# Performance work log

Hardware: AMD Instinct MI355X
Metric: run time of the kernel (lower is better)

Reference implementation:

```python
import jax, jax.numpy as jnp
import numpy as np

S, B, D, H, E, HID = 512, 16, 768, 12, 8, 3072
HD = D // H
EPS = 1e-5


def _ln(x, w, b):
    m = jnp.mean(x, axis=-1, keepdims=True)
    v = jnp.var(x, axis=-1, keepdims=True)
    return (x - m) * jax.lax.rsqrt(v + EPS) * w + b


def setup_inputs() -> dict:
    key = jax.random.key(0)
    ks = jax.random.split(key, 9)
    n = lambda k, *sh: jax.random.normal(k, sh, dtype=jnp.float32) * 0.02
    return dict(
        x=jax.random.normal(ks[0], (S, B, D), dtype=jnp.float32),
        ln1_w=jnp.ones((D,), jnp.float32), ln1_b=jnp.zeros((D,), jnp.float32),
        wq=n(ks[1], D, D), bq=jnp.zeros((D,), jnp.float32),
        wk=n(ks[2], D, D), bk=jnp.zeros((D,), jnp.float32),
        wv=n(ks[3], D, D), bv=jnp.zeros((D,), jnp.float32),
        wo=n(ks[4], D, D), bo=jnp.zeros((D,), jnp.float32),
        ln2_w=jnp.ones((D,), jnp.float32), ln2_b=jnp.zeros((D,), jnp.float32),
        wg=n(ks[5], D, E), bg=jnp.zeros((E,), jnp.float32),
        w1=n(ks[6], E, D, HID), b1=jnp.zeros((E, HID), jnp.float32),
        w2=n(ks[7], E, HID, D), b2=jnp.zeros((E, D), jnp.float32),
    )


def _block(x, ln1_w, ln1_b, wq, bq, wk, bk, wv, bv, wo, bo,
           ln2_w, ln2_b, wg, bg, w1, b1, w2, b2):
    # --- attention: source uses query = norm1(x), key = value = x ---
    q_in = _ln(x, ln1_w, ln1_b)
    q = (q_in @ wq + bq).reshape(S, B, H, HD)
    k = (x @ wk + bk).reshape(S, B, H, HD)
    v = (x @ wv + bv).reshape(S, B, H, HD)
    scores = jnp.einsum('sbhd,tbhd->bhst', q, k) * (1.0 / HD ** 0.5)
    p = jax.nn.softmax(scores, axis=-1)
    attn = jnp.einsum('bhst,tbhd->sbhd', p, v).reshape(S, B, D)
    x = x + attn @ wo + bo
    # --- top-1 MoE MLP on norm2(x) ---
    t = _ln(x, ln2_w, ln2_b).reshape(S * B, D)   # [T, D] routed tokens
    logits = t @ wg + bg                          # [T, E]
    probs = jax.nn.softmax(logits, axis=-1)
    idx = jnp.argmax(logits, axis=-1)             # top-1 expert per token
    gate = jnp.take_along_axis(probs, idx[:, None], axis=-1)   # [T, 1]
    comb = jax.nn.one_hot(idx, E, dtype=t.dtype) * gate        # [T, E]

    def expert(w1e, b1e, w2e, b2e):
        return jax.nn.gelu(t @ w1e + b1e, approximate=False) @ w2e + b2e

    y = jax.vmap(expert)(w1, b1, w2, b2)          # [E, T, D]
    moe = jnp.einsum('te,etd->td', comb, y).reshape(S, B, D)
    return x + moe


def reference(x, ln1_w, ln1_b, wq, bq, wk, bk, wv, bv, wo, bo,
              ln2_w, ln2_b, wg, bg, w1, b1, w2, b2):
    return _block(x, ln1_w, ln1_b, wq, bq, wk, bk, wv, bv, wo, bo,
                  ln2_w, ln2_b, wg, bg, w1, b1, w2, b2)
```

## Files before the change

kernel.cpp:

```cpp
#include <hip/hip_runtime.h>
#include <math.h>

#define SS 512
#define BB 16
#define DD 768
#define HH 12
#define HDIM 64
#define EE 8
#define HID 3072
#define TT 8192
#define EPSV 1e-5f
#define KVSTR 1536
#define ASTR 72
#define NBANK 64

typedef __attribute__((ext_vector_type(8))) short s16x8;
typedef __attribute__((ext_vector_type(4))) short s16x4;
typedef __attribute__((ext_vector_type(4))) float f32x4;

__device__ inline short f2bf(float f) {
  unsigned u = __builtin_bit_cast(unsigned, f);
  unsigned r = (u + 0x7fffu + ((u >> 16) & 1u)) >> 16;
  return (short)r;
}

__device__ inline float gelu_f(float x) {
  float y = 0.7978845608028654f * (x + 0.044715f * x * x * x);
  float e = __expf(2.f * y);
  float t = 1.f - 2.f / (e + 1.f);
  return 0.5f * x * (1.f + t);
}

__device__ inline void gl2lds16(const void* g, void* l) {
  __builtin_amdgcn_global_load_lds(
      (const __attribute__((address_space(1))) unsigned int*)g,
      (__attribute__((address_space(3))) unsigned int*)l, 16, 0, 0);
}

__global__ __launch_bounds__(256) void transpose4_bf16(const float* __restrict__ w0,
    const float* __restrict__ w1p, const float* __restrict__ w2p,
    const float* __restrict__ w3p, short* __restrict__ dst) {
  const int z = blockIdx.z;
  const float* W = (z == 0) ? w0 : (z == 1) ? w1p : (z == 2) ? w2p : w3p;
  short* Wt = dst + (size_t)z * DD * DD;
  int k0 = blockIdx.x * 64, n0 = blockIdx.y * 64;
  __shared__ float t[64][65];
  for (int i = threadIdx.x; i < 1024; i += 256) {
    int r = i >> 4, c4 = (i & 15) << 2;
    const float4 v = *(const float4*)(W + (size_t)(k0 + r) * DD + n0 + c4);
    t[r][c4] = v.x; t[r][c4 + 1] = v.y; t[r][c4 + 2] = v.z; t[r][c4 + 3] = v.w;
  }
  __syncthreads();
  for (int i = threadIdx.x; i < 1024; i += 256) {
    int r = i >> 4, c4 = (i & 15) << 2;
    s16x4 sv;
    sv.x = f2bf(t[c4][r]);     sv.y = f2bf(t[c4 + 1][r]);
    sv.z = f2bf(t[c4 + 2][r]); sv.w = f2bf(t[c4 + 3][r]);
    *(s16x4*)(Wt + (size_t)(n0 + r) * DD + k0 + c4) = sv;
  }
}

__global__ __launch_bounds__(256) void transpose_bf16(const float* __restrict__ W,
    short* __restrict__ Wt, int K, int N) {
  const float* Wz = W + (size_t)blockIdx.z * K * N;
  short* Wtz = Wt + (size_t)blockIdx.z * K * N;
  int k0 = blockIdx.x * 64, n0 = blockIdx.y * 64;
  __shared__ float t[64][65];
  for (int i = threadIdx.x; i < 1024; i += 256) {
    int r = i >> 4, c4 = (i & 15) << 2;
    const float4 v = *(const float4*)(Wz + (size_t)(k0 + r) * N + n0 + c4);
    t[r][c4] = v.x; t[r][c4 + 1] = v.y; t[r][c4 + 2] = v.z; t[r][c4 + 3] = v.w;
  }
  __syncthreads();
  for (int i = threadIdx.x; i < 1024; i += 256) {
    int r = i >> 4, c4 = (i & 15) << 2;
    s16x4 sv;
    sv.x = f2bf(t[c4][r]);     sv.y = f2bf(t[c4 + 1][r]);
    sv.z = f2bf(t[c4 + 2][r]); sv.w = f2bf(t[c4 + 3][r]);
    *(s16x4*)(Wtz + (size_t)(n0 + r) * K + k0 + c4) = sv;
  }
}

__global__ __launch_bounds__(256) void gate_transpose(const float* __restrict__ wg,
    float* __restrict__ wgT) {
  for (int i = threadIdx.x + blockIdx.x * 256; i < EE * DD; i += 256 * 8) {
    int e = i / DD, d = i - e * DD;
    wgT[i] = wg[d * EE + e];
  }
}

__global__ __launch_bounds__(256) void fused_cvt_ln1(const float* __restrict__ x,
    const float* __restrict__ w, const float* __restrict__ b,
    short* __restrict__ xbf, short* __restrict__ ln1bf) {
  const int tok = blockIdx.x * 4 + (threadIdx.x >> 6);
  const int lane = threadIdx.x & 63;
  const float* row = x + (size_t)tok * DD;
  const float4 v0 = *(const float4*)(row + lane * 4);
  const float4 v1 = *(const float4*)(row + 256 + lane * 4);
  const float4 v2 = *(const float4*)(row + 512 + lane * 4);
  float s = v0.x + v0.y + v0.z + v0.w + v1.x + v1.y + v1.z + v1.w
          + v2.x + v2.y + v2.z + v2.w;
  float ss = v0.x * v0.x + v0.y * v0.y + v0.z * v0.z + v0.w * v0.w
           + v1.x * v1.x + v1.y * v1.y + v1.z * v1.z + v1.w * v1.w
           + v2.x * v2.x + v2.y * v2.y + v2.z * v2.z + v2.w * v2.w;
#pragma unroll
  for (int o = 1; o < 64; o <<= 1) { s += __shfl_xor(s, o); ss += __shfl_xor(ss, o); }
  const float mean = s * (1.f / DD);
  const float inv = rsqrtf(ss * (1.f / DD) - mean * mean + EPSV);
  short* xrow = xbf + (size_t)tok * DD;
  short* lrow = ln1bf + (size_t)tok * DD;
#define LN1_CHUNK(v, off) { \
  const float4 wv = *(const float4*)(w + (off) + lane * 4); \
  const float4 bv = *(const float4*)(b + (off) + lane * 4); \
  s16x4 xa, la; \
  xa.x = f2bf(v.x); xa.y = f2bf(v.y); xa.z = f2bf(v.z); xa.w = f2bf(v.w); \
  la.x = f2bf((v.x - mean) * inv * wv.x + bv.x); \
  la.y = f2bf((v.y - mean) * inv * wv.y + bv.y); \
  la.z = f2bf((v.z - mean) * inv * wv.z + bv.z); \
  la.w = f2bf((v.w - mean) * inv * wv.w + bv.w); \
  *(s16x4*)(xrow + (off) + lane * 4) = xa; \
  *(s16x4*)(lrow + (off) + lane * 4) = la; }
  LN1_CHUNK(v0, 0)
  LN1_CHUNK(v1, 256)
  LN1_CHUNK(v2, 512)
#undef LN1_CHUNK
}

__global__ __launch_bounds__(256) void fused_ln2_route(const float* __restrict__ x1,
    const float* __restrict__ w, const float* __restrict__ b,
    const float* __restrict__ wgT, const float* __restrict__ bg,
    short* __restrict__ tlnbf, int* __restrict__ idx, float* __restrict__ gate,
    int* __restrict__ cnt2) {
  const int tok = blockIdx.x * 4 + (threadIdx.x >> 6);
  const int lane = threadIdx.x & 63;
  const float* row = x1 + (size_t)tok * DD;
  const float4 v0 = *(const float4*)(row + lane * 4);
  const float4 v1 = *(const float4*)(row + 256 + lane * 4);
  const float4 v2 = *(const float4*)(row + 512 + lane * 4);
  float s = v0.x + v0.y + v0.z + v0.w + v1.x + v1.y + v1.z + v1.w
          + v2.x + v2.y + v2.z + v2.w;
  float ss = v0.x * v0.x + v0.y * v0.y + v0.z * v0.z + v0.w * v0.w
           + v1.x * v1.x + v1.y * v1.y + v1.z * v1.z + v1.w * v1.w
           + v2.x * v2.x + v2.y * v2.y + v2.z * v2.z + v2.w * v2.w;
#pragma unroll
  for (int o = 1; o < 64; o <<= 1) { s += __shfl_xor(s, o); ss += __shfl_xor(ss, o); }
  const float mean = s * (1.f / DD);
  const float inv = rsqrtf(ss * (1.f / DD) - mean * mean + EPSV);
  short* srow = tlnbf + (size_t)tok * DD;
  float acc[EE];
#pragma unroll
  for (int e = 0; e < EE; ++e) acc[e] = 0.f;
#define LN2_CHUNK(v, off) { \
  const float4 wv = *(const float4*)(w + (off) + lane * 4); \
  const float4 bv = *(const float4*)(b + (off) + lane * 4); \
  float4 n; \
  n.x = (v.x - mean) * inv * wv.x + bv.x; \
  n.y = (v.y - mean) * inv * wv.y + bv.y; \
  n.z = (v.z - mean) * inv * wv.z + bv.z; \
  n.w = (v.w - mean) * inv * wv.w + bv.w; \
  s16x4 sv; sv.x = f2bf(n.x); sv.y = f2bf(n.y); sv.z = f2bf(n.z); sv.w = f2bf(n.w); \
  *(s16x4*)(srow + (off) + lane * 4) = sv; \
  const int i0 = (off) + lane * 4; \
  _Pragma("unroll") \
  for (int e = 0; e < EE; ++e) { \
    const float4 g = *(const float4*)(wgT + (size_t)e * DD + i0); \
    acc[e] += n.x * g.x + n.y * g.y + n.z * g.z + n.w * g.w; } }
  LN2_CHUNK(v0, 0)
  LN2_CHUNK(v1, 256)
  LN2_CHUNK(v2, 512)
#undef LN2_CHUNK
#pragma unroll
  for (int o = 1; o < 64; o <<= 1)
#pragma unroll
    for (int e = 0; e < EE; ++e) acc[e] += __shfl_xor(acc[e], o);
  if (lane == 0) {
#pragma unroll
    for (int e = 0; e < EE; ++e) acc[e] += bg[e];
    int best = 0; float bm = acc[0];
#pragma unroll
    for (int e = 1; e < EE; ++e) if (acc[e] > bm) { bm = acc[e]; best = e; }
    float sum = 0.f;
#pragma unroll
    for (int e = 0; e < EE; ++e) sum += __expf(acc[e] - bm);
    idx[tok] = best;
    gate[tok] = 1.0f / sum;
    atomicAdd(&cnt2[(blockIdx.x & (NBANK - 1)) * 16 + best], 1);
  }
}

__global__ void prefix2_kernel(const int* __restrict__ cnt2, int* __restrict__ cnt,
                               int* __restrict__ off, int* __restrict__ tb,
                               int* __restrict__ bankbase) {
  const int lane = threadIdx.x;
  int c[EE], excl[EE], tot[EE];
#pragma unroll
  for (int e = 0; e < EE; ++e) c[e] = cnt2[lane * 16 + e];
#pragma unroll
  for (int e = 0; e < EE; ++e) {
    int x = c[e];
#pragma unroll
    for (int o = 1; o < 64; o <<= 1) {
      int y = __shfl_up(x, o);
      if (lane >= o) x += y;
    }
    excl[e] = x - c[e];
    tot[e] = __shfl(x, 63);
  }
  int oo = 0;
  int offl[EE];
#pragma unroll
  for (int e = 0; e < EE; ++e) { offl[e] = oo; oo += tot[e]; }
#pragma unroll
  for (int e = 0; e < EE; ++e)
    bankbase[lane * EE + e] = offl[e] + excl[e];
  if (lane == 0) {
    int o = 0, t = 0;
    for (int e = 0; e < EE; ++e) {
      off[e] = o; tb[e] = t; cnt[e] = tot[e];
      o += tot[e]; t += (tot[e] + 127) >> 7;
    }
    off[EE] = o; tb[EE] = t;
  }
}

__global__ __launch_bounds__(256) void scatter_kernel(const int* __restrict__ idx,
    const int* __restrict__ bankbase, int* __restrict__ cur2, int* __restrict__ perm) {
  int t = blockIdx.x * 256 + threadIdx.x;
  if (t < TT) {
    int e = idx[t];
    int bank = (t >> 2) & (NBANK - 1);
    int p = atomicAdd(&cur2[bank * 16 + e], 1);
    perm[bankbase[bank * EE + e] + p] = t;
  }
}

template<int MODE, int OUTBF, int COLS>
__global__ __launch_bounds__(256) void mgemm(const short* __restrict__ A,
    const short* __restrict__ Wt, const float* __restrict__ bias,
    const float* __restrict__ bias2, const float* __restrict__ res,
    void* __restrict__ C, int N, int K) {
  const int bx = blockIdx.x;
  const int lid = bx >> 3;
  const int colt = lid >> 3, rband = lid & 7;
  const int bm = (((bx & 7) << 3) + rband) * 128;
  const int bn = colt * COLS;
  constexpr int NJ = COLS / 32;
  __shared__ short As[128 * 32];
  __shared__ short Bs[COLS * 32];
  const int tid = threadIdx.x;
  const int wave = tid >> 6, lane = tid & 63;
  const int wr = (wave >> 1) * 64, wc = (wave & 1) * (COLS / 2);
  const int l16 = lane & 15, quad = lane >> 4;
  const int kq = (((lane & 3) ^ ((lane >> 3) & 3)) << 3);
  const int sw = ((l16 >> 1) & 3);
  const short* Ab = A + (size_t)(bm + (wave << 5) + (lane >> 2)) * K + kq;
  const short* Bb = Wt + (size_t)(bn + wave * (COLS / 4) + (lane >> 2)) * K + kq;
  short* lA = &As[(wave << 5) * 32];
  short* lB = &Bs[wave * (COLS / 4) * 32];
  f32x4 acc[4][NJ] = {};
  for (int k0 = 0; k0 < K; k0 += 32) {
    gl2lds16(Ab + k0, lA);
    gl2lds16(Ab + (size_t)16 * K + k0, lA + 512);
    gl2lds16(Bb + k0, lB);
    if (COLS == 128) gl2lds16(Bb + (size_t)16 * K + k0, lB + 512);
    __syncthreads();
    s16x8 af[4], bfr[NJ];
#pragma unroll
    for (int i = 0; i < 4; ++i)
      af[i] = *(s16x8*)(&As[(wr + i * 16 + l16) * 32 + ((quad ^ sw) << 3)]);
#pragma unroll
    for (int j = 0; j < NJ; ++j)
      bfr[j] = *(s16x8*)(&Bs[(wc + j * 16 + l16) * 32 + ((quad ^ sw) << 3)]);
#pragma unroll
    for (int i = 0; i < 4; ++i)
#pragma unroll
      for (int j = 0; j < NJ; ++j)
        acc[i][j] = __builtin_amdgcn_mfma_f32_16x16x32_bf16(af[i], bfr[j], acc[i][j], 0, 0, 0);
    __syncthreads();
  }
#pragma unroll
  for (int i = 0; i < 4; ++i) {
#pragma unroll
    for (int r = 0; r < 4; ++r) {
      int row = bm + wr + i * 16 + quad * 4 + r;
#pragma unroll
      for (int j = 0; j < NJ; ++j) {
        int col = bn + wc + j * 16 + l16;
        float bv = (MODE == 2) ? (col >= DD ? bias2[col - DD] : bias[col]) : bias[col];
        float val = acc[i][j][r] + bv;
        if (MODE == 1) val += res[(size_t)row * N + col];
        if (OUTBF) ((short*)C)[(size_t)row * N + col] = f2bf(val);
        else       ((float*)C)[(size_t)row * N + col] = val;
      }
    }
  }
}

__global__ __launch_bounds__(256) void qkv_mgemm(const short* __restrict__ ln1bf,
    const short* __restrict__ xbf, const short* __restrict__ wqT,
    const short* __restrict__ kvT, const float* __restrict__ bq,
    const float* __restrict__ bk, const float* __restrict__ bv,
    short* __restrict__ qbf, short* __restrict__ kvbf) {
  const int bx = blockIdx.x;
  const int lid = bx >> 3;
  const int colt = lid >> 3, rband = lid & 7;
  const int bm = (((bx & 7) << 3) + rband) * 128;
  const bool isQ = (colt < 6);
  const int bn = isQ ? colt * 128 : (colt - 6) * 128;
  const short* A  = isQ ? ln1bf : xbf;
  const short* Bt = isQ ? wqT : kvT;
  const float* bias = isQ ? bq : (bn < DD ? bk : bv);
  const int bofs = (!isQ && bn >= DD) ? DD : 0;
  short* out = isQ ? qbf : kvbf;
  const int OS = isQ ? DD : KVSTR;
  const int K = DD;
  __shared__ short As[128 * 32];
  __shared__ short Bs[128 * 32];
  const int tid = threadIdx.x;
  const int wave = tid >> 6, lane = tid & 63;
  const int wr = (wave >> 1) * 64, wc = (wave & 1) * 64;
  const int l16 = lane & 15, quad = lane >> 4;
  const int kq = (((lane & 3) ^ ((lane >> 3) & 3)) << 3);
  const int sw = ((l16 >> 1) & 3);
  const short* Ab = A + (size_t)(bm + (wave << 5) + (lane >> 2)) * K + kq;
  const short* Bb = Bt + (size_t)(bn + (wave << 5) + (lane >> 2)) * K + kq;
  short* lA = &As[(wave << 5) * 32];
  short* lB = &Bs[(wave << 5) * 32];
  f32x4 acc[4][4] = {};
  for (int k0 = 0; k0 < K; k0 += 32) {
    gl2lds16(Ab + k0, lA);
    gl2lds16(Ab + (size_t)16 * K + k0, lA + 512);
    gl2lds16(Bb + k0, lB);
    gl2lds16(Bb + (size_t)16 * K + k0, lB + 512);
    __syncthreads();
    s16x8 af[4], bfr[4];
#pragma unroll
    for (int i = 0; i < 4; ++i)
      af[i] = *(s16x8*)(&As[(wr + i * 16 + l16) * 32 + ((quad ^ sw) << 3)]);
#pragma unroll
    for (int j = 0; j < 4; ++j)
      bfr[j] = *(s16x8*)(&Bs[(wc + j * 16 + l16) * 32 + ((quad ^ sw) << 3)]);
#pragma unroll
    for (int i = 0; i < 4; ++i)
#pragma unroll
      for (int j = 0; j < 4; ++j)
        acc[i][j] = __builtin_amdgcn_mfma_f32_16x16x32_bf16(af[i], bfr[j], acc[i][j], 0, 0, 0);
    __syncthreads();
  }
#pragma unroll
  for (int i = 0; i < 4; ++i) {
#pragma unroll
    for (int r = 0; r < 4; ++r) {
      int row = bm + wr + i * 16 + quad * 4 + r;
#pragma unroll
      for (int j = 0; j < 4; ++j) {
        int col = bn + wc + j * 16 + l16;
        float val = acc[i][j][r] + bias[col - bofs];
        out[(size_t)row * OS + col] = f2bf(val);
      }
    }
  }
}

__global__ __launch_bounds__(256) void attn_mfma(const short* __restrict__ q,
    const short* __restrict__ k, const short* __restrict__ v, short* __restrict__ o) {
  const int qt = blockIdx.x, bidx = blockIdx.y, hidx = blockIdx.z;
  const int tid = threadIdx.x;
  const int wave = tid >> 6, lane = tid & 63;
  const int l16 = lane & 15, quad = lane >> 4;
  const int s0 = qt * 64;
  __shared__ short Qs[64 * ASTR];
  __shared__ short Ks[64 * ASTR];
  __shared__ short Vs[64 * ASTR];
  __shared__ short Ps[64 * ASTR];
  for (int i = tid; i < 512; i += 256) {
    int r = i >> 3, c8 = i & 7;
    *(s16x8*)(&Qs[r * ASTR + c8 * 8]) =
        *(const s16x8*)(q + ((size_t)(s0 + r) * BB + bidx) * DD + hidx * HDIM + c8 * 8);
  }
  __syncthreads();
  s16x8 af0 = *(s16x8*)(&Qs[(wave * 16 + l16) * ASTR + quad * 8]);
  s16x8 af1 = *(s16x8*)(&Qs[(wave * 16 + l16) * ASTR + 32 + quad * 8]);
  f32x4 oacc[4] = {};
  float mr[4], lr[4];
#pragma unroll
  for (int r = 0; r < 4; ++r) { mr[r] = -1e30f; lr[r] = 0.f; }

  for (int t0 = 0; t0 < SS; t0 += 64) {
    __syncthreads();
    for (int i = tid; i < 512; i += 256) {
      int r = i >> 3, c8 = i & 7;
      *(s16x8*)(&Ks[r * ASTR + c8 * 8]) =
          *(const s16x8*)(k + ((size_t)(t0 + r) * BB + bidx) * KVSTR + hidx * HDIM + c8 * 8);
    }
    for (int i = tid; i < 1024; i += 256) {
      int r = i >> 4, c4 = i & 15;
      s16x4 vv = *(const s16x4*)(v + ((size_t)(t0 + r) * BB + bidx) * KVSTR + hidx * HDIM + c4 * 4);
      Vs[(c4 * 4 + 0) * ASTR + r] = vv.x;
      Vs[(c4 * 4 + 1) * ASTR + r] = vv.y;
      Vs[(c4 * 4 + 2) * ASTR + r] = vv.z;
      Vs[(c4 * 4 + 3) * ASTR + r] = vv.w;
    }
    __syncthreads();
    f32x4 sc[4];
    const f32x4 zero = {};
#pragma unroll
    for (int j = 0; j < 4; ++j) {
      s16x8 kf0 = *(s16x8*)(&Ks[(j * 16 + l16) * ASTR + quad * 8]);
      s16x8 kf1 = *(s16x8*)(&Ks[(j * 16 + l16) * ASTR + 32 + quad * 8]);
      sc[j] = __builtin_amdgcn_mfma_f32_16x16x32_bf16(af0, kf0, zero, 0, 0, 0);
      sc[j] = __builtin_amdgcn_mfma_f32_16x16x32_bf16(af1, kf1, sc[j], 0, 0, 0);
#pragma unroll
      for (int r = 0; r < 4; ++r) sc[j][r] *= 0.125f;
    }
    float tm[4], alpha[4], rs[4];
#pragma unroll
    for (int r = 0; r < 4; ++r) {
      tm[r] = mr[r];
#pragma unroll
      for (int j = 0; j < 4; ++j) tm[r] = fmaxf(tm[r], sc[j][r]);
    }
#pragma unroll
    for (int mask = 1; mask < 16; mask <<= 1)
#pragma unroll
      for (int r = 0; r < 4; ++r) tm[r] = fmaxf(tm[r], __shfl_xor(tm[r], mask));
#pragma unroll
    for (int r = 0; r < 4; ++r) { alpha[r] = __expf(mr[r] - tm[r]); mr[r] = tm[r]; rs[r] = 0.f; }
#pragma unroll
    for (int j = 0; j < 4; ++j)
#pragma unroll
      for (int r = 0; r < 4; ++r) {
        float p = __expf(sc[j][r] - tm[r]);
        sc[j][r] = p; rs[r] += p;
      }
#pragma unroll
    for (int mask = 1; mask < 16; mask <<= 1)
#pragma unroll
      for (int r = 0; r < 4; ++r) rs[r] += __shfl_xor(rs[r], mask);
#pragma unroll
    for (int r = 0; r < 4; ++r) lr[r] = lr[r] * alpha[r] + rs[r];
#pragma unroll
    for (int j = 0; j < 4; ++j)
#pragma unroll
      for (int r = 0; r < 4; ++r)
        Ps[(wave * 16 + quad * 4 + r) * ASTR + j * 16 + l16] = f2bf(sc[j][r]);
#pragma unroll
    for (int jd = 0; jd < 4; ++jd)
#pragma unroll
      for (int r = 0; r < 4; ++r) oacc[jd][r] *= alpha[r];
    __syncthreads();
    s16x8 pf0 = *(s16x8*)(&Ps[(wave * 16 + l16) * ASTR + quad * 8]);
    s16x8 pf1 = *(s16x8*)(&Ps[(wave * 16 + l16) * ASTR + 32 + quad * 8]);
#pragma unroll
    for (int jd = 0; jd < 4; ++jd) {
      s16x8 vf0 = *(s16x8*)(&Vs[(jd * 16 + l16) * ASTR + quad * 8]);
      s16x8 vf1 = *(s16x8*)(&Vs[(jd * 16 + l16) * ASTR + 32 + quad * 8]);
      oacc[jd] = __builtin_amdgcn_mfma_f32_16x16x32_bf16(pf0, vf0, oacc[jd], 0, 0, 0);
      oacc[jd] = __builtin_amdgcn_mfma_f32_16x16x32_bf16(pf1, vf1, oacc[jd], 0, 0, 0);
    }
  }
#pragma unroll
  for (int r = 0; r < 4; ++r) {
    int row = s0 + wave * 16 + quad * 4 + r;
    float invl = 1.f / lr[r];
#pragma unroll
    for (int jd = 0; jd < 4; ++jd) {
      int d = jd * 16 + l16;
      o[((size_t)row * BB + bidx) * DD + hidx * HDIM + d] = f2bf(oacc[jd][r] * invl);
    }
  }
}

__global__ __launch_bounds__(512) void egemm1(const short* __restrict__ tlnbf,
    const short* __restrict__ w1t, const float* __restrict__ b1,
    const int* __restrict__ off, const int* __restrict__ tb, const int* __restrict__ cnt,
    const int* __restrict__ perm, short* __restrict__ hbuf) {
  const int bx = blockIdx.x;
  const int lid = bx >> 3;
  const int rband = lid % 9, colt = lid / 9;
  const int row = (bx & 7) * 9 + rband;
  if (row >= tb[EE]) return;
  int e = 0;
  while (e < EE - 1 && tb[e + 1] <= row) ++e;
  const int lt = row - tb[e];
  const int cnte = cnt[e];
  const int slot0 = off[e] + lt * 128;
  const int slast = off[e] + cnte - 1;
  const int bn = colt * 128;
  const int tid = threadIdx.x;
  const int wave = tid >> 6, lane = tid & 63;
  const int wr = (wave >> 2) * 64;
  const int wc = (wave & 3) * 32;
  const int l16 = lane & 15, quad = lane >> 4;
  const int kq = (((lane & 3) ^ ((lane >> 3) & 3)) << 3);
  const int sw = ((l16 >> 1) & 3);
  __shared__ short As[128 * 32];
  __shared__ short Bs[128 * 32];
  f32x4 acc[4][2] = {};
  const int sA = slot0 + (wave << 4) + (lane >> 2);
  const int tokA = perm[sA <= slast ? sA : slast];
  const short* AbA = tlnbf + (size_t)tokA * DD + kq;
  const short* Bb = w1t + (size_t)e * DD * HID
                  + (size_t)(bn + (wave << 4) + (lane >> 2)) * DD + kq;
  short* lA = &As[(wave << 4) * 32];
  short* lB = &Bs[(wave << 4) * 32];
  for (int k0 = 0; k0 < DD; k0 += 32) {
    gl2lds16(AbA + k0, lA);
    gl2lds16(Bb + k0, lB);
    __syncthreads();
    s16x8 af[4], bfr[2];
#pragma unroll
    for (int i = 0; i < 4; ++i)
      af[i] = *(s16x8*)(&As[(wr + i * 16 + l16) * 32 + ((quad ^ sw) << 3)]);
#pragma unroll
    for (int j = 0; j < 2; ++j)
      bfr[j] = *(s16x8*)(&Bs[(wc + j * 16 + l16) * 32 + ((quad ^ sw) << 3)]);
#pragma unroll
    for (int i = 0; i < 4; ++i)
#pragma unroll
      for (int j = 0; j < 2; ++j)
        acc[i][j] = __builtin_amdgcn_mfma_f32_16x16x32_bf16(af[i], bfr[j], acc[i][j], 0, 0, 0);
    __syncthreads();
  }
#pragma unroll
  for (int i = 0; i < 4; ++i) {
#pragma unroll
    for (int r = 0; r < 4; ++r) {
      int rl = wr + i * 16 + quad * 4 + r;
      if (lt * 128 + rl >= cnte) continue;
#pragma unroll
      for (int j = 0; j < 2; ++j) {
        int col = bn + wc + j * 16 + l16;
        float xv = acc[i][j][r] + b1[e * HID + col];
        hbuf[(size_t)(slot0 + rl) * HID + col] = f2bf(gelu_f(xv));
      }
    }
  }
}

__global__ __launch_bounds__(256) void egemm2(const short* __restrict__ hbuf,
    const short* __restrict__ w2t, const float* __restrict__ b2,
    const int* __restrict__ perm, const int* __restrict__ off,
    const int* __restrict__ tb, const int* __restrict__ cnt,
    const float* __restrict__ gate, const float* __restrict__ x1,
    float* __restrict__ out) {
  const int bx = blockIdx.x;
  const int lid = bx >> 3;
  const int colt = lid % 12, rband = lid / 12;
  const int row = (bx & 7) * 9 + rband;
  if (row >= tb[EE]) return;
  int e = 0;
  while (e < EE - 1 && tb[e + 1] <= row) ++e;
  const int lt = row - tb[e];
  const int cnte = cnt[e];
  const int slot0 = off[e] + lt * 128;
  const int bn = colt * 64;
  const int tid = threadIdx.x;
  const int wave = tid >> 6, lane = tid & 63;
  const int wr = (wave >> 1) * 64, wc = (wave & 1) * 32;
  const int l16 = lane & 15, quad = lane >> 4;
  const int rg = lane >> 3;
  const int kq8 = (((lane & 7) ^ rg) << 3);
  const int swz = l16 & 7;
  __shared__ short As[128 * 64];
  __shared__ short Bs[64 * 64];
  __shared__ int stok[128];
  if (tid < 128) stok[tid] = (lt * 128 + tid < cnte) ? perm[slot0 + tid] : -1;
  f32x4 acc[4][2] = {};
  const short* Ab = hbuf + (size_t)(slot0 + (wave << 5) + rg) * HID + kq8;
  const short* Bb = w2t + (size_t)e * HID * DD
                  + (size_t)(bn + wave * 16 + rg) * HID + kq8;
  short* lA = &As[(wave << 5) * 64];
  short* lB = &Bs[wave * 16 * 64];
  for (int k0 = 0; k0 < HID; k0 += 64) {
    gl2lds16(Ab + k0, lA);
    gl2lds16(Ab + (size_t)8 * HID + k0, lA + 512);
    gl2lds16(Ab + (size_t)16 * HID + k0, lA + 1024);
    gl2lds16(Ab + (size_t)24 * HID + k0, lA + 1536);
    gl2lds16(Bb + k0, lB);
    gl2lds16(Bb + (size_t)8 * HID + k0, lB + 512);
    __syncthreads();
#pragma unroll
    for (int h = 0; h < 2; ++h) {
      s16x8 af[4], bfr[2];
#pragma unroll
      for (int i = 0; i < 4; ++i)
        af[i] = *(s16x8*)(&As[(wr + i * 16 + l16) * 64 + (((quad + 4 * h) ^ swz) << 3)]);
#pragma unroll
      for (int j = 0; j < 2; ++j)
        bfr[j] = *(s16x8*)(&Bs[(wc + j * 16 + l16) * 64 + (((quad + 4 * h) ^ swz) << 3)]);
#pragma unroll
      for (int i = 0; i < 4; ++i)
#pragma unroll
        for (int j = 0; j < 2; ++j)
          acc[i][j] = __builtin_amdgcn_mfma_f32_16x16x32_bf16(af[i], bfr[j], acc[i][j], 0, 0, 0);
    }
    __syncthreads();
  }
#pragma unroll
  for (int i = 0; i < 4; ++i) {
#pragma unroll
    for (int r = 0; r < 4; ++r) {
      int rl = wr + i * 16 + quad * 4 + r;
      if (lt * 128 + rl >= cnte) continue;
      int tok = stok[rl];
      float g = gate[tok];
#pragma unroll
      for (int j = 0; j < 2; ++j) {
        int col = bn + wc + j * 16 + l16;
        float val = acc[i][j][r] + b2[e * DD + col];
        out[(size_t)tok * DD + col] = x1[(size_t)tok * DD + col] + g * val;
      }
    }
  }
}

extern "C" void kernel_launch(void* const* d_in, const int* in_sizes, int n_in,
                              void* d_out, int out_size, void* d_ws, size_t ws_size,
                              hipStream_t stream) {
  const float* x     = (const float*)d_in[0];
  const float* ln1_w = (const float*)d_in[1];
  const float* ln1_b = (const float*)d_in[2];
  const float* wq    = (const float*)d_in[3];
  const float* bq    = (const float*)d_in[4];
  const float* wk    = (const float*)d_in[5];
  const float* bk    = (const float*)d_in[6];
  const float* wv    = (const float*)d_in[7];
  const float* bv    = (const float*)d_in[8];
  const float* wo    = (const float*)d_in[9];
  const float* bo    = (const float*)d_in[10];
  const float* ln2_w = (const float*)d_in[11];
  const float* ln2_b = (const float*)d_in[12];
  const float* wg    = (const float*)d_in[13];
  const float* bg    = (const float*)d_in[14];
  const float* w1    = (const float*)d_in[15];
  const float* b1    = (const float*)d_in[16];
  const float* w2    = (const float*)d_in[17];
  const float* b2    = (const float*)d_in[18];
  float* out = (float*)d_out;
  float* ws = (float*)d_ws;

  const size_t TD = (size_t)TT * DD;
  float* x1    = ws;
  short* tlnbf = (short*)(ws + TD);
  short* sbase = (short*)(ws + 2 * TD);
  short* xbf   = sbase;
  short* ln1bf = sbase + TD + 128 * DD;
  short* attbf = ln1bf;
  short* qbf   = ln1bf + TD;
  short* kvbf  = qbf + TD;
  short* hbuf  = kvbf + (size_t)TT * KVSTR;
  short* wqT   = hbuf + (size_t)(TT + 128) * HID;
  short* kvT   = wqT + (size_t)DD * DD;
  short* woT   = kvT + (size_t)KVSTR * DD;
  short* w1T   = woT + (size_t)DD * DD;
  short* w2T   = w1T + (size_t)EE * DD * HID;
  int*   meta  = (int*)(w2T + (size_t)EE * HID * DD);
  int*   idx   = meta;
  float* gate  = (float*)(meta + TT);
  int*   perm  = meta + 2 * TT;
  int*   cnt2  = meta + 3 * TT;
  int*   cur2  = cnt2 + NBANK * 16;
  int*   bankbase = cur2 + NBANK * 16;
  int*   cnt   = bankbase + NBANK * EE;
  int*   off   = cnt + 8;
  int*   tb    = off + 9;
  float* wgT   = (float*)(tb + 9);

  hipMemsetAsync(cnt2, 0, 2 * NBANK * 16 * sizeof(int), stream);

  transpose4_bf16<<<dim3(12, 12, 4), 256, 0, stream>>>(wq, wk, wv, wo, wqT);
  transpose_bf16<<<dim3(12, 48, 8), 256, 0, stream>>>(w1, w1T, DD, HID);
  transpose_bf16<<<dim3(48, 12, 8), 256, 0, stream>>>(w2, w2T, HID, DD);
  gate_transpose<<<8, 256, 0, stream>>>(wg, wgT);

  fused_cvt_ln1<<<TT / 4, 256, 0, stream>>>(x, ln1_w, ln1_b, xbf, ln1bf);

  qkv_mgemm<<<8 * 8 * 18, 256, 0, stream>>>(ln1bf, xbf, wqT, kvT, bq, bk, bv, qbf, kvbf);

  attn_mfma<<<dim3(SS / 64, BB, HH), 256, 0, stream>>>(qbf, kvbf, kvbf + DD, attbf);

  mgemm<1, 0, 64><<<64 * 12, 256, 0, stream>>>(attbf, woT, bo, nullptr, x, x1, DD, DD);

  fused_ln2_route<<<TT / 4, 256, 0, stream>>>(x1, ln2_w, ln2_b, wgT, bg,
                                              tlnbf, idx, gate, cnt2);
  prefix2_kernel<<<1, 64, 0, stream>>>(cnt2, cnt, off, tb, bankbase);
  scatter_kernel<<<TT / 256, 256, 0, stream>>>(idx, bankbase, cur2, perm);

  egemm1<<<8 * 9 * 24, 512, 0, stream>>>(tlnbf, w1T, b1, off, tb, cnt, perm, hbuf);
  egemm2<<<8 * 9 * 12, 256, 0, stream>>>(hbuf, w2T, b2, perm, off, tb, cnt, gate, x1, out);
}
```

Measured before the change: 553.6 us.

## Deepen K-step to 64 and use 8 waves in QKV and expert GEMM1

The QKV GEMM changes from 4 waves to 8 waves per block, with each wave computing a 64x32 sub-tile. Both the QKV GEMM and the first expert GEMM now stage 64-wide K slices in LDS instead of 32, using an 8-way XOR swizzle. This halves the number of K iterations and barriers per tile and raises in-flight waves per block. In exchange, LDS use per block doubles, which may reduce how many blocks fit per CU.

```diff
diff --git a/kernel.cpp b/kernel.cpp
--- a/kernel.cpp
+++ b/kernel.cpp
@@ -296,7 +296,7 @@
   }
 }
 
-__global__ __launch_bounds__(256) void qkv_mgemm(const short* __restrict__ ln1bf,
+__global__ __launch_bounds__(512) void qkv_mgemm(const short* __restrict__ ln1bf,
     const short* __restrict__ xbf, const short* __restrict__ wqT,
     const short* __restrict__ kvT, const float* __restrict__ bq,
     const float* __restrict__ bk, const float* __restrict__ bv,
@@ -314,37 +314,42 @@
   short* out = isQ ? qbf : kvbf;
   const int OS = isQ ? DD : KVSTR;
   const int K = DD;
-  __shared__ short As[128 * 32];
-  __shared__ short Bs[128 * 32];
+  __shared__ short As[128 * 64];
+  __shared__ short Bs[128 * 64];
   const int tid = threadIdx.x;
   const int wave = tid >> 6, lane = tid & 63;
-  const int wr = (wave >> 1) * 64, wc = (wave & 1) * 64;
+  const int wr = (wave >> 2) * 64;
+  const int wc = (wave & 3) * 32;
   const int l16 = lane & 15, quad = lane >> 4;
-  const int kq = (((lane & 3) ^ ((lane >> 3) & 3)) << 3);
-  const int sw = ((l16 >> 1) & 3);
-  const short* Ab = A + (size_t)(bm + (wave << 5) + (lane >> 2)) * K + kq;
-  const short* Bb = Bt + (size_t)(bn + (wave << 5) + (lane >> 2)) * K + kq;
-  short* lA = &As[(wave << 5) * 32];
-  short* lB = &Bs[(wave << 5) * 32];
-  f32x4 acc[4][4] = {};
-  for (int k0 = 0; k0 < K; k0 += 32) {
+  const int rg = lane >> 3;
+  const int kq8 = (((lane & 7) ^ rg) << 3);
+  const int swz = l16 & 7;
+  const short* Ab = A + (size_t)(bm + (wave << 4) + rg) * K + kq8;
+  const short* Bb = Bt + (size_t)(bn + (wave << 4) + rg) * K + kq8;
+  short* lA = &As[(wave << 4) * 64];
+  short* lB = &Bs[(wave << 4) * 64];
+  f32x4 acc[4][2] = {};
+  for (int k0 = 0; k0 < K; k0 += 64) {
     gl2lds16(Ab + k0, lA);
-    gl2lds16(Ab + (size_t)16 * K + k0, lA + 512);
+    gl2lds16(Ab + (size_t)8 * K + k0, lA + 512);
     gl2lds16(Bb + k0, lB);
-    gl2lds16(Bb + (size_t)16 * K + k0, lB + 512);
-    __syncthreads();
-    s16x8 af[4], bfr[4];
-#pragma unroll
-    for (int i = 0; i < 4; ++i)
-      af[i] = *(s16x8*)(&As[(wr + i * 16 + l16) * 32 + ((quad ^ sw) << 3)]);
-#pragma unroll
-    for (int j = 0; j < 4; ++j)
-      bfr[j] = *(s16x8*)(&Bs[(wc + j * 16 + l16) * 32 + ((quad ^ sw) << 3)]);
-#pragma unroll
-    for (int i = 0; i < 4; ++i)
-#pragma unroll
-      for (int j = 0; j < 4; ++j)
-        acc[i][j] = __builtin_amdgcn_mfma_f32_16x16x32_bf16(af[i], bfr[j], acc[i][j], 0, 0, 0);
+    gl2lds16(Bb + (size_t)8 * K + k0, lB + 512);
+    __syncthreads();
+#pragma unroll
+    for (int h = 0; h < 2; ++h) {
+      s16x8 af[4], bfr[2];
+#pragma unroll
+      for (int i = 0; i < 4; ++i)
+        af[i] = *(s16x8*)(&As[(wr + i * 16 + l16) * 64 + (((quad + 4 * h) ^ swz) << 3)]);
+#pragma unroll
+      for (int j = 0; j < 2; ++j)
+        bfr[j] = *(s16x8*)(&Bs[(wc + j * 16 + l16) * 64 + (((quad + 4 * h) ^ swz) << 3)]);
+#pragma unroll
+      for (int i = 0; i < 4; ++i)
+#pragma unroll
+        for (int j = 0; j < 2; ++j)
+          acc[i][j] = __builtin_amdgcn_mfma_f32_16x16x32_bf16(af[i], bfr[j], acc[i][j], 0, 0, 0);
+    }
     __syncthreads();
   }
 #pragma unroll
@@ -353,7 +358,7 @@
     for (int r = 0; r < 4; ++r) {
       int row = bm + wr + i * 16 + quad * 4 + r;
 #pragma unroll
-      for (int j = 0; j < 4; ++j) {
+      for (int j = 0; j < 2; ++j) {
         int col = bn + wc + j * 16 + l16;
         float val = acc[i][j][r] + bias[col - bofs];
         out[(size_t)row * OS + col] = f2bf(val);
@@ -492,34 +497,42 @@
   const int wr = (wave >> 2) * 64;
   const int wc = (wave & 3) * 32;
   const int l16 = lane & 15, quad = lane >> 4;
-  const int kq = (((lane & 3) ^ ((lane >> 3) & 3)) << 3);
-  const int sw = ((l16 >> 1) & 3);
-  __shared__ short As[128 * 32];
-  __shared__ short Bs[128 * 32];
+  const int rg = lane >> 3;
+  const int kq8 = (((lane & 7) ^ rg) << 3);
+  const int swz = l16 & 7;
+  __shared__ short As[128 * 64];
+  __shared__ short Bs[128 * 64];
   f32x4 acc[4][2] = {};
-  const int sA = slot0 + (wave << 4) + (lane >> 2);
-  const int tokA = perm[sA <= slast ? sA : slast];
-  const short* AbA = tlnbf + (size_t)tokA * DD + kq;
+  const int sA0 = slot0 + (wave << 4) + rg;
+  const int tokA = perm[sA0 <= slast ? sA0 : slast];
+  const int tokB = perm[(sA0 + 8) <= slast ? (sA0 + 8) : slast];
+  const short* AbA = tlnbf + (size_t)tokA * DD + kq8;
+  const short* AbB = tlnbf + (size_t)tokB * DD + kq8;
   const short* Bb = w1t + (size_t)e * DD * HID
-                  + (size_t)(bn + (wave << 4) + (lane >> 2)) * DD + kq;
-  short* lA = &As[(wave << 4) * 32];
-  short* lB = &Bs[(wave << 4) * 32];
-  for (int k0 = 0; k0 < DD; k0 += 32) {
+                  + (size_t)(bn + (wave << 4) + rg) * DD + kq8;
+  short* lA = &As[(wave << 4) * 64];
+  short* lB = &Bs[(wave << 4) * 64];
+  for (int k0 = 0; k0 < DD; k0 += 64) {
     gl2lds16(AbA + k0, lA);
+    gl2lds16(AbB + k0, lA + 512);
     gl2lds16(Bb + k0, lB);
-    __syncthreads();
-    s16x8 af[4], bfr[2];
-#pragma unroll
-    for (int i = 0; i < 4; ++i)
-      af[i] = *(s16x8*)(&As[(wr + i * 16 + l16) * 32 + ((quad ^ sw) << 3)]);
-#pragma unroll
-    for (int j = 0; j < 2; ++j)
-      bfr[j] = *(s16x8*)(&Bs[(wc + j * 16 + l16) * 32 + ((quad ^ sw) << 3)]);
-#pragma unroll
-    for (int i = 0; i < 4; ++i)
+    gl2lds16(Bb + (size_t)8 * DD + k0, lB + 512);
+    __syncthreads();
+#pragma unroll
+    for (int h = 0; h < 2; ++h) {
+      s16x8 af[4], bfr[2];
+#pragma unroll
+      for (int i = 0; i < 4; ++i)
+        af[i] = *(s16x8*)(&As[(wr + i * 16 + l16) * 64 + (((quad + 4 * h) ^ swz) << 3)]);
 #pragma unroll
       for (int j = 0; j < 2; ++j)
-        acc[i][j] = __builtin_amdgcn_mfma_f32_16x16x32_bf16(af[i], bfr[j], acc[i][j], 0, 0, 0);
+        bfr[j] = *(s16x8*)(&Bs[(wc + j * 16 + l16) * 64 + (((quad + 4 * h) ^ swz) << 3)]);
+#pragma unroll
+      for (int i = 0; i < 4; ++i)
+#pragma unroll
+        for (int j = 0; j < 2; ++j)
+          acc[i][j] = __builtin_amdgcn_mfma_f32_16x16x32_bf16(af[i], bfr[j], acc[i][j], 0, 0, 0);
+    }
     __syncthreads();
   }
 #pragma unroll
@@ -676,7 +689,7 @@
 
   fused_cvt_ln1<<<TT / 4, 256, 0, stream>>>(x, ln1_w, ln1_b, xbf, ln1bf);
 
-  qkv_mgemm<<<8 * 8 * 18, 256, 0, stream>>>(ln1bf, xbf, wqT, kvT, bq, bk, bv, qbf, kvbf);
+  qkv_mgemm<<<8 * 8 * 18, 512, 0, stream>>>(ln1bf, xbf, wqT, kvT, bq, bk, bv, qbf, kvbf);
 
   attn_mfma<<<dim3(SS / 64, BB, HH), 256, 0, stream>>>(qbf, kvbf, kvbf + DD, attbf);
 
```

New measurement: 539.9 us. -2.5%, faster.
